# Kernel optimization log

Hardware: AMD Instinct MI355X
Metric: run time of the kernel (lower is better)

## Reference

```python
import jax, jax.numpy as jnp
import numpy as np

HID, NH_FULL, K, GAMMA = 768, 12, 9, 2
HD = HID // NH_FULL            # 64
NH = NH_FULL // GAMMA          # 6
RH = HD * NH                   # 384 reduced hidden dim
OUT_HALF = HID // 2            # 384
B, S = 8, 1024


def setup_inputs() -> dict:
    key0 = jax.random.key(0)
    ks = jax.random.split(key0, 20)
    r = lambda i, shape, sc=0.02: (jax.random.normal(ks[i], shape, dtype=jnp.float32) * sc)
    inp = {
        'query': jax.random.normal(ks[0], (B, S, HID), dtype=jnp.float32),
        'mask': jnp.ones((B, 1, 1, S), dtype=jnp.int32),
        # q/k/v projections: hidden -> reduced
        'Wq': r(1, (HID, RH)), 'bq': jnp.zeros((RH,), jnp.float32),
        'Wk': r(2, (HID, RH)), 'bk': jnp.zeros((RH,), jnp.float32),
        'Wv': r(3, (HID, RH)), 'bv': jnp.zeros((RH,), jnp.float32),
        # depthwise separable conv: depthwise [HID,1,K] + pointwise [RH,HID]
        'dw_w': r(4, (HID, 1, K), 0.1), 'dw_b': jnp.zeros((HID,), jnp.float32),
        'pw_w': r(5, (RH, HID)), 'pw_b': jnp.zeros((RH,), jnp.float32),
        # self-attn output proj: reduced -> hidden//2
        'Wsa': r(6, (RH, OUT_HALF)), 'bsa': jnp.zeros((OUT_HALF,), jnp.float32),
        # dynamic kernel layer: reduced -> K*NH
        'Wdk': r(7, (RH, K * NH)), 'bdk': jnp.zeros((K * NH,), jnp.float32),
        # dynamic attn output proj: reduced -> hidden//2
        'Wda': r(8, (RH, OUT_HALF)), 'bda': jnp.zeros((OUT_HALF,), jnp.float32),
    }
    # self_attn=True requires query==key==value
    inp['key'] = inp['query']
    inp['value'] = inp['query']
    return inp


def _forward(query, key, value, mask, Wq, bq, Wk, bk, Wv, bv,
             dw_w, dw_b, pw_w, pw_b, Wsa, bsa, Wdk, bdk, Wda, bda):
    b, s, _ = query.shape
    q = query @ Wq + bq          # [B,S,RH]
    k = key @ Wk + bk
    v = value @ Wv + bv

    # ---- depthwise separable conv over key (seq axis), 'same' padding ----
    key_t = jnp.transpose(key, (0, 2, 1))  # [B,HID,S]
    dw = jax.lax.conv_general_dilated(
        key_t, dw_w, window_strides=(1,), padding=[(K // 2, K // 2)],
        feature_group_count=HID, dimension_numbers=('NCH', 'OIH', 'NCH'))
    dw = dw + dw_b[None, :, None]          # [B,HID,S]
    ks_feat = jnp.einsum('bhs,rh->bsr', dw, pw_w) + pw_b  # [B,S,RH]

    # ---- standard multi-head self-attention branch ----
    def split(x):  # [B,S,RH] -> [B,NH,S,HD]
        return x.reshape(b, s, NH, HD).transpose(0, 2, 1, 3)
    qh, kh, vh = split(q), split(k), split(v)
    scores = jnp.einsum('bhqd,bhkd->bhqk', qh, kh) / jnp.sqrt(jnp.float32(HD))
    scores = jnp.where(mask == 0, jnp.float32(-jnp.inf), scores)
    attn_wts = jax.nn.softmax(scores, axis=-1)             # [B,NH,S,S]
    attn_out = jnp.einsum('bhqk,bhkd->bhqd', attn_wts, vh)
    attn_out = attn_out.transpose(0, 2, 1, 3).reshape(b, s, RH)
    self_out = attn_out @ Wsa + bsa                         # [B,S,HID//2]

    # ---- span dynamic conv attention branch ----
    # unfold v into sliding windows: expanded[b,s,h,d,k] = v_pad[b, s+k, h*HD+d]
    v_pad = jnp.pad(v, ((0, 0), (K // 2, K // 2), (0, 0)))  # [B,S+K-1,RH]
    windows = jnp.stack([v_pad[:, i:i + s] for i in range(K)], axis=-1)  # [B,S,RH,K]
    windows = windows.reshape(b, s, NH, HD, K)
    dyn_logits = (q * ks_feat) @ Wdk + bdk                  # [B,S,K*NH]
    dyn_kernel = jax.nn.softmax(dyn_logits.reshape(b, s, NH, K), axis=-1)
    dyn_out = jnp.einsum('bshdk,bshk->bshd', windows, dyn_kernel).reshape(b, s, RH)
    dyn_out = dyn_out @ Wda + bda                           # [B,S,HID//2]

    return attn_wts, jnp.concatenate([self_out, dyn_out], axis=-1)


def reference(query, key, value, mask, Wq, bq, Wk, bk, Wv, bv,
              dw_w, dw_b, pw_w, pw_b, Wsa, bsa, Wdk, bdk, Wda, bda):
    return _forward(query, key, value, mask, Wq, bq, Wk, bk, Wv, bv,
                    dw_w, dw_b, pw_w, pw_b, Wsa, bsa, Wdk, bdk, Wda, bda)
```

## Files before the change

### kernel.cpp

```cpp
#include <hip/hip_runtime.h>
#include <math.h>

#define B 8
#define S 1024
#define HID 768
#define RH 384
#define NH 6
#define HD 64
#define KW 9
#define KNH 54
#define OUTHALF 384
#define QLD 1152
#define EXPSCALE 0.18033688f

typedef __attribute__((ext_vector_type(8))) short short8;
typedef __attribute__((ext_vector_type(4))) float f32x4;

#define SWZ(r, c) (((r) << 6) + ((c) ^ (((r) & 7) << 3)))

__device__ __forceinline__ ushort f2bf(float x) {
    unsigned u = __float_as_uint(x);
    u += 0x7FFF + ((u >> 16) & 1);
    return (ushort)(u >> 16);
}
__device__ __forceinline__ float bf2f(ushort u) {
    return __uint_as_float(((unsigned)u) << 16);
}
__device__ __forceinline__ short8 cvt8(const float* p) {
    short8 r;
    #pragma unroll
    for (int i = 0; i < 8; i++) r[i] = (short)f2bf(p[i]);
    return r;
}

__global__ __launch_bounds__(256) void cvt_dw_fused(
    const float* __restrict__ query, const float* __restrict__ dw_w,
    const float* __restrict__ dw_b, ushort* __restrict__ Xbf,
    ushort* __restrict__ dwout)
{
    int idx = blockIdx.x*256 + threadIdx.x;
    if (idx >= B*S*(HID/8)) return;
    int c0 = (idx % (HID/8))*8;
    int s  = (idx / (HID/8)) % S;
    int b  = idx / ((HID/8)*S);

    float ctr[8];
    *(float4*)&ctr[0] = *(const float4*)(query + ((size_t)b*S + s)*HID + c0);
    *(float4*)&ctr[4] = *(const float4*)(query + ((size_t)b*S + s)*HID + c0 + 4);
    *(short8*)(Xbf + ((size_t)b*S + s)*HID + c0) = cvt8(ctr);

    float acc[8];
    *(float4*)&acc[0] = *(const float4*)(dw_b + c0);
    *(float4*)&acc[4] = *(const float4*)(dw_b + c0 + 4);
    #pragma unroll
    for (int kk = 0; kk < KW; kk++) {
        int sp = s + kk - KW/2;
        if (sp >= 0 && sp < S) {
            float row[8];
            *(float4*)&row[0] = *(const float4*)(query + ((size_t)b*S + sp)*HID + c0);
            *(float4*)&row[4] = *(const float4*)(query + ((size_t)b*S + sp)*HID + c0 + 4);
            #pragma unroll
            for (int j = 0; j < 8; j++)
                acc[j] += row[j] * dw_w[(c0+j)*KW + kk];
        }
    }
    *(short8*)(dwout + ((size_t)b*S + s)*HID + c0) = cvt8(acc);
}

__global__ __launch_bounds__(256) void prep_weights(
    const float* __restrict__ Wq, const float* __restrict__ Wk, const float* __restrict__ Wv,
    const float* __restrict__ bq, const float* __restrict__ bk, const float* __restrict__ bv,
    const float* __restrict__ pw_w, const float* __restrict__ Wsa,
    const float* __restrict__ Wda, const float* __restrict__ Wdk,
    ushort* __restrict__ WqkvT, ushort* __restrict__ pw_bf,
    ushort* __restrict__ WsaT, ushort* __restrict__ WdaT, ushort* __restrict__ WdkT,
    float* __restrict__ bqkv)
{
    int i = blockIdx.x*256 + threadIdx.x;
    if (i < 884736) {
        int n = i / 768, kk = i % 768;
        int w = n / 384, nn = n % 384;
        const float* W = (w == 0) ? Wq : (w == 1) ? Wk : Wv;
        WqkvT[i] = f2bf(W[kk*384 + nn]);
        return;
    }
    i -= 884736;
    if (i < 294912) { pw_bf[i] = f2bf(pw_w[i]); return; }
    i -= 294912;
    if (i < 147456) {
        int n = i / 384, kk = i % 384;
        WsaT[i] = f2bf(Wsa[kk*384 + n]);
        return;
    }
    i -= 147456;
    if (i < 147456) {
        int n = i / 384, kk = i % 384;
        WdaT[i] = f2bf(Wda[kk*384 + n]);
        return;
    }
    i -= 147456;
    if (i < 49152) {
        int n = i / 384, kk = i % 384;
        WdkT[i] = (n < KNH) ? f2bf(Wdk[kk*KNH + n]) : (ushort)0;
        return;
    }
    i -= 49152;
    if (i < 1152) {
        bqkv[i] = (i < 384) ? bq[i] : (i < 768) ? bk[i-384] : bv[i-768];
    }
}

template<bool OUTBF>
__global__ __launch_bounds__(256) void gemm_mfma(
    const ushort* __restrict__ A, const ushort* __restrict__ Bt,
    const float* __restrict__ bias, void* __restrict__ Cout,
    int N, int Kd, int ldc)
{
    __shared__ __attribute__((aligned(16))) ushort As[128*32];
    __shared__ __attribute__((aligned(16))) ushort Bs[128*32];
    const int t = threadIdx.x;
    const int wave = t >> 6, lane = t & 63;
    const int lr = lane & 15, lg = lane >> 4;
    const int wr = wave >> 1, wc = wave & 1;
    const int bm = blockIdx.y * 128, bn = blockIdx.x * 128;

    f32x4 acc[4][4] = {};
    const int srow = t >> 1, sseg = t & 1;
    const ushort* Arow = A + (size_t)(bm + srow)*Kd + sseg*16;
    const ushort* Brow = Bt + (size_t)(bn + srow)*Kd + sseg*16;
    const int g0 = (sseg*2) ^ (srow & 3), g1 = (sseg*2 + 1) ^ (srow & 3);
    const int swz = lg ^ (lr & 3);

    short8 av0 = *(const short8*)(Arow);
    short8 av1 = *(const short8*)(Arow + 8);
    short8 bv0 = *(const short8*)(Brow);
    short8 bv1 = *(const short8*)(Brow + 8);

    for (int k0 = 0; k0 < Kd; k0 += 32) {
        __syncthreads();
        *(short8*)&As[srow*32 + g0*8] = av0;
        *(short8*)&As[srow*32 + g1*8] = av1;
        *(short8*)&Bs[srow*32 + g0*8] = bv0;
        *(short8*)&Bs[srow*32 + g1*8] = bv1;
        __syncthreads();
        if (k0 + 32 < Kd) {
            av0 = *(const short8*)(Arow + k0 + 32);
            av1 = *(const short8*)(Arow + k0 + 40);
            bv0 = *(const short8*)(Brow + k0 + 32);
            bv1 = *(const short8*)(Brow + k0 + 40);
        }
        short8 af[4], bfr[4];
        #pragma unroll
        for (int m = 0; m < 4; m++)
            af[m] = *(const short8*)&As[(wr*64 + m*16 + lr)*32 + swz*8];
        #pragma unroll
        for (int n = 0; n < 4; n++)
            bfr[n] = *(const short8*)&Bs[(wc*64 + n*16 + lr)*32 + swz*8];
        #pragma unroll
        for (int m = 0; m < 4; m++)
            #pragma unroll
            for (int n = 0; n < 4; n++)
                acc[m][n] = __builtin_amdgcn_mfma_f32_16x16x32_bf16(af[m], bfr[n], acc[m][n], 0, 0, 0);
    }

    #pragma unroll
    for (int m = 0; m < 4; m++) {
        #pragma unroll
        for (int n = 0; n < 4; n++) {
            int gcol = bn + wc*64 + n*16 + lr;
            if (gcol >= N) continue;
            float bz = bias[gcol];
            #pragma unroll
            for (int r = 0; r < 4; r++) {
                size_t grow = bm + wr*64 + m*16 + lg*4 + r;
                float val = acc[m][n][r] + bz;
                if (OUTBF) ((ushort*)Cout)[grow*ldc + gcol] = f2bf(val);
                else       ((float*)Cout)[grow*ldc + gcol] = val;
            }
        }
    }
}

template<bool OUTBF, bool DUAL>
__global__ __launch_bounds__(256) void gemm64(
    const ushort* __restrict__ A0, const ushort* __restrict__ Bt0,
    const float* __restrict__ bias0, void* __restrict__ C0,
    const ushort* __restrict__ A1, const ushort* __restrict__ Bt1,
    const float* __restrict__ bias1,
    int N, int Kd, int ldc)
{
    __shared__ __attribute__((aligned(16))) ushort As[64*32];
    __shared__ __attribute__((aligned(16))) ushort Bs[64*32];
    const ushort* A  = (DUAL && blockIdx.z) ? A1 : A0;
    const ushort* Bt = (DUAL && blockIdx.z) ? Bt1 : Bt0;
    const float* bias = (DUAL && blockIdx.z) ? bias1 : bias0;
    const int coff = (DUAL && blockIdx.z) ? OUTHALF : 0;

    const int t = threadIdx.x;
    const int wave = t >> 6, lane = t & 63;
    const int lr = lane & 15, lg = lane >> 4;
    const int wr = wave >> 1, wc = wave & 1;
    const int bm = blockIdx.y * 64, bn = blockIdx.x * 64;

    f32x4 acc[2][2] = {};
    const int srow = t >> 2, sseg = t & 3;
    const ushort* Arow = A + (size_t)(bm + srow)*Kd + sseg*8;
    const ushort* Brow = Bt + (size_t)(bn + srow)*Kd + sseg*8;
    const int gs = sseg ^ (srow & 3);
    const int swz = lg ^ (lr & 3);

    short8 av = *(const short8*)(Arow);
    short8 bv = *(const short8*)(Brow);

    for (int k0 = 0; k0 < Kd; k0 += 32) {
        __syncthreads();
        *(short8*)&As[srow*32 + gs*8] = av;
        *(short8*)&Bs[srow*32 + gs*8] = bv;
        __syncthreads();
        if (k0 + 32 < Kd) {
            av = *(const short8*)(Arow + k0 + 32);
            bv = *(const short8*)(Brow + k0 + 32);
        }
        short8 af[2], bfr[2];
        #pragma unroll
        for (int m = 0; m < 2; m++)
            af[m] = *(const short8*)&As[(wr*32 + m*16 + lr)*32 + swz*8];
        #pragma unroll
        for (int n = 0; n < 2; n++)
            bfr[n] = *(const short8*)&Bs[(wc*32 + n*16 + lr)*32 + swz*8];
        #pragma unroll
        for (int m = 0; m < 2; m++)
            #pragma unroll
            for (int n = 0; n < 2; n++)
                acc[m][n] = __builtin_amdgcn_mfma_f32_16x16x32_bf16(af[m], bfr[n], acc[m][n], 0, 0, 0);
    }

    #pragma unroll
    for (int m = 0; m < 2; m++) {
        #pragma unroll
        for (int n = 0; n < 2; n++) {
            int gcol = bn + wc*32 + n*16 + lr;
            if (gcol >= N) continue;
            float bz = bias[gcol];
            #pragma unroll
            for (int r = 0; r < 4; r++) {
                size_t grow = bm + wr*32 + m*16 + lg*4 + r;
                float val = acc[m][n][r] + bz;
                if (OUTBF) ((ushort*)C0)[grow*ldc + gcol + coff] = f2bf(val);
                else       ((float*)C0)[grow*ldc + gcol + coff] = val;
            }
        }
    }
}

__global__ __launch_bounds__(64) void gemm_qksdk(
    const ushort* __restrict__ qkv, const ushort* __restrict__ ksf,
    const ushort* __restrict__ WdkT, const float* __restrict__ bdk,
    float* __restrict__ dynlog)
{
    const int lane = threadIdx.x;
    const int lr = lane & 15, lg = lane >> 4;
    const int r0 = blockIdx.x * 16;
    const int row = r0 + lr;

    f32x4 acc[4] = {};
    for (int ks = 0; ks < RH/32; ks++) {
        int k0 = ks*32 + lg*8;
        short8 qv = *(const short8*)(qkv + (size_t)row*QLD + k0);
        short8 kv = *(const short8*)(ksf + (size_t)row*RH + k0);
        short8 afr;
        #pragma unroll
        for (int j = 0; j < 8; j++)
            afr[j] = (short)f2bf(bf2f((ushort)qv[j]) * bf2f((ushort)kv[j]));
        #pragma unroll
        for (int t4 = 0; t4 < 4; t4++) {
            short8 bfr = *(const short8*)(WdkT + (size_t)(t4*16 + lr)*RH + k0);
            acc[t4] = __builtin_amdgcn_mfma_f32_16x16x32_bf16(afr, bfr, acc[t4], 0, 0, 0);
        }
    }
    #pragma unroll
    for (int t4 = 0; t4 < 4; t4++) {
        int n = t4*16 + lr;
        if (n >= KNH) continue;
        float bz = bdk[n];
        #pragma unroll
        for (int r = 0; r < 4; r++)
            dynlog[(size_t)(r0 + lg*4 + r)*KNH + n] = acc[t4][r] + bz;
    }
}

__global__ __launch_bounds__(256) void attn_fused(
    const ushort* __restrict__ qkv, const int* __restrict__ mask,
    float* __restrict__ out0, ushort* __restrict__ attnws)
{
    __shared__ __attribute__((aligned(16))) ushort Ks[64*64];
    __shared__ __attribute__((aligned(16))) ushort Vt[64*64];
    __shared__ __attribute__((aligned(16))) ushort Ps[4][16*64];

    const int b = blockIdx.z, h = blockIdx.y, q0 = blockIdx.x * 64;
    const int t = threadIdx.x;
    const int wave = t >> 6, lane = t & 63;
    const int lr = lane & 15, lg = lane >> 4;

    const ushort* qrow = qkv + (size_t)(b*S + q0 + wave*16 + lr)*QLD + h*HD;
    short8 aQ0 = *(const short8*)(qrow + lg*8);
    short8 aQ1 = *(const short8*)(qrow + 32 + lg*8);

    const int srow = t >> 2;
    const int sseg = t & 3;
    const int* mrow = mask + b*S;
    const ushort* krbase = qkv + RH + (size_t)(b*S + srow)*QLD + h*HD + sseg*16;
    const ushort* vbase  = qkv + 2*RH + (size_t)b*S*QLD + h*HD + srow;

    float lsum[4] = {0.f, 0.f, 0.f, 0.f};

    short8 kv0 = *(const short8*)(krbase);
    short8 kv1 = *(const short8*)(krbase + 8);
    for (int kc = 0; kc < S; kc += 64) {
        __syncthreads();
        *(short8*)&Ks[SWZ(srow, sseg*16)]     = kv0;
        *(short8*)&Ks[SWZ(srow, sseg*16 + 8)] = kv1;
        __syncthreads();
        if (kc + 64 < S) {
            const ushort* kr = krbase + (size_t)(kc + 64)*QLD;
            kv0 = *(const short8*)(kr);
            kv1 = *(const short8*)(kr + 8);
        }
        #pragma unroll
        for (int t4 = 0; t4 < 4; t4++) {
            short8 b0 = *(const short8*)&Ks[SWZ(t4*16 + lr, lg*8)];
            short8 b1 = *(const short8*)&Ks[SWZ(t4*16 + lr, 32 + lg*8)];
            f32x4 c = {0.f, 0.f, 0.f, 0.f};
            c = __builtin_amdgcn_mfma_f32_16x16x32_bf16(aQ0, b0, c, 0, 0, 0);
            c = __builtin_amdgcn_mfma_f32_16x16x32_bf16(aQ1, b1, c, 0, 0, 0);
            float add = mrow[kc + t4*16 + lr] ? 0.f : -1e30f;
            #pragma unroll
            for (int r = 0; r < 4; r++)
                lsum[r] += exp2f(c[r]*EXPSCALE + add);
        }
    }
    #pragma unroll
    for (int r = 0; r < 4; r++) {
        #pragma unroll
        for (int off = 1; off < 16; off <<= 1)
            lsum[r] += __shfl_xor(lsum[r], off, 16);
    }
    float inv[4];
    #pragma unroll
    for (int r = 0; r < 4; r++) inv[r] = 1.f / lsum[r];

    f32x4 o[4] = {};
    ushort* Psw = &Ps[wave][0];
    const size_t obase = ((size_t)((b*NH + h)*S) + q0 + wave*16) * (size_t)S;

    kv0 = *(const short8*)(krbase);
    kv1 = *(const short8*)(krbase + 8);
    ushort vb[16];
    #pragma unroll
    for (int i = 0; i < 16; i++)
        vb[i] = vbase[(size_t)(sseg*16 + i)*QLD];

    for (int kc = 0; kc < S; kc += 64) {
        __syncthreads();
        *(short8*)&Ks[SWZ(srow, sseg*16)]     = kv0;
        *(short8*)&Ks[SWZ(srow, sseg*16 + 8)] = kv1;
        *(short8*)&Vt[SWZ(srow, sseg*16)]     = *(short8*)&vb[0];
        *(short8*)&Vt[SWZ(srow, sseg*16 + 8)] = *(short8*)&vb[8];
        __syncthreads();
        if (kc + 64 < S) {
            const ushort* kr = krbase + (size_t)(kc + 64)*QLD;
            kv0 = *(const short8*)(kr);
            kv1 = *(const short8*)(kr + 8);
            const ushort* vp = vbase + (size_t)(kc + 64)*QLD;
            #pragma unroll
            for (int i = 0; i < 16; i++)
                vb[i] = vp[(size_t)(sseg*16 + i)*QLD];
        }

        #pragma unroll
        for (int t4 = 0; t4 < 4; t4++) {
            short8 b0 = *(const short8*)&Ks[SWZ(t4*16 + lr, lg*8)];
            short8 b1 = *(const short8*)&Ks[SWZ(t4*16 + lr, 32 + lg*8)];
            f32x4 c = {0.f, 0.f, 0.f, 0.f};
            c = __builtin_amdgcn_mfma_f32_16x16x32_bf16(aQ0, b0, c, 0, 0, 0);
            c = __builtin_amdgcn_mfma_f32_16x16x32_bf16(aQ1, b1, c, 0, 0, 0);
            float add = mrow[kc + t4*16 + lr] ? 0.f : -1e30f;
            #pragma unroll
            for (int r = 0; r < 4; r++) {
                float p = exp2f(c[r]*EXPSCALE + add) * inv[r];
                __builtin_nontemporal_store(p, &out0[obase + (size_t)(lg*4 + r)*S + kc + t4*16 + lr]);
                Psw[SWZ(lg*4 + r, t4*16 + lr)] = f2bf(p);
            }
        }
        #pragma unroll
        for (int kh = 0; kh < 2; kh++) {
            short8 pa = *(const short8*)&Psw[SWZ(lr, kh*32 + lg*8)];
            #pragma unroll
            for (int dt = 0; dt < 4; dt++) {
                short8 vv = *(const short8*)&Vt[SWZ(dt*16 + lr, kh*32 + lg*8)];
                o[dt] = __builtin_amdgcn_mfma_f32_16x16x32_bf16(pa, vv, o[dt], 0, 0, 0);
            }
        }
    }

    #pragma unroll
    for (int dt = 0; dt < 4; dt++)
        #pragma unroll
        for (int r = 0; r < 4; r++)
            attnws[(size_t)(b*S + q0 + wave*16 + lg*4 + r)*RH + h*HD + dt*16 + lr] = f2bf(o[dt][r]);
}

__global__ __launch_bounds__(256) void dyn_conv(
    const float* __restrict__ logits, const ushort* __restrict__ qkv,
    ushort* __restrict__ dynout)
{
    int idx = blockIdx.x*256 + threadIdx.x;
    if (idx >= B*S*(RH/4)) return;
    int r4 = (idx % (RH/4))*4;
    int s  = (idx / (RH/4)) % S;
    int b  = idx / ((RH/4)*S);
    int h  = r4 / HD;
    const float* lg = logits + ((size_t)b*S + s)*KNH + h*KW;
    float mx = lg[0];
    #pragma unroll
    for (int kk = 1; kk < KW; kk++) mx = fmaxf(mx, lg[kk]);
    float e[KW], sum = 0.f;
    #pragma unroll
    for (int kk = 0; kk < KW; kk++) { e[kk] = __expf(lg[kk]-mx); sum += e[kk]; }
    float inv = 1.f/sum;
    float acc[4] = {0.f, 0.f, 0.f, 0.f};
    const ushort* vbase = qkv + 2*RH;
    #pragma unroll
    for (int kk = 0; kk < KW; kk++) {
        int sp = s + kk - KW/2;
        if (sp >= 0 && sp < S) {
            const ushort* vp = vbase + (size_t)(b*S + sp)*QLD + r4;
            #pragma unroll
            for (int j = 0; j < 4; j++) acc[j] += bf2f(vp[j]) * e[kk];
        }
    }
    ushort4 o;
    o.x = f2bf(acc[0]*inv); o.y = f2bf(acc[1]*inv);
    o.z = f2bf(acc[2]*inv); o.w = f2bf(acc[3]*inv);
    *(ushort4*)(dynout + ((size_t)b*S + s)*RH + r4) = o;
}

extern "C" void kernel_launch(void* const* d_in, const int* in_sizes, int n_in,
                              void* d_out, int out_size, void* d_ws, size_t ws_size,
                              hipStream_t stream) {
    const float* query = (const float*)d_in[0];
    const int*   mask  = (const int*)d_in[1];
    const float* Wq    = (const float*)d_in[2];
    const float* bq    = (const float*)d_in[3];
    const float* Wk    = (const float*)d_in[4];
    const float* bk    = (const float*)d_in[5];
    const float* Wv    = (const float*)d_in[6];
    const float* bv    = (const float*)d_in[7];
    const float* dw_w  = (const float*)d_in[8];
    const float* dw_b  = (const float*)d_in[9];
    const float* pw_w  = (const float*)d_in[10];
    const float* pw_b  = (const float*)d_in[11];
    const float* Wsa   = (const float*)d_in[12];
    const float* bsa   = (const float*)d_in[13];
    const float* Wdk   = (const float*)d_in[14];
    const float* bdk   = (const float*)d_in[15];
    const float* Wda   = (const float*)d_in[16];
    const float* bda   = (const float*)d_in[17];

    float* out0 = (float*)d_out;
    float* out1 = out0 + (size_t)B*NH*S*S;

    char* wsb = (char*)d_ws;
    size_t off = 0;
    auto alloc = [&](size_t bytes) { char* p = wsb + off; off += (bytes + 255) & ~255ull; return p; };
    ushort* Xbf    = (ushort*)alloc((size_t)B*S*HID*2);
    ushort* qkvbf  = (ushort*)alloc((size_t)B*S*QLD*2);
    ushort* dwbf   = (ushort*)alloc((size_t)B*S*HID*2);
    ushort* ksf    = (ushort*)alloc((size_t)B*S*RH*2);
    ushort* attnbf = (ushort*)alloc((size_t)B*S*RH*2);
    ushort* dynbf  = (ushort*)alloc((size_t)B*S*RH*2);
    float*  dynlog = (float*) alloc((size_t)B*S*KNH*4);
    ushort* WqkvT  = (ushort*)alloc((size_t)QLD*HID*2);
    ushort* pw_bf  = (ushort*)alloc((size_t)RH*HID*2);
    ushort* WsaT   = (ushort*)alloc((size_t)RH*RH*2);
    ushort* WdaT   = (ushort*)alloc((size_t)RH*RH*2);
    ushort* WdkT   = (ushort*)alloc((size_t)128*RH*2);
    float*  bqkv   = (float*) alloc((size_t)QLD*4);

    const int M = B*S;

    prep_weights<<<(1524864 + 255)/256, 256, 0, stream>>>(
        Wq, Wk, Wv, bq, bk, bv, pw_w, Wsa, Wda, Wdk,
        WqkvT, pw_bf, WsaT, WdaT, WdkT, bqkv);

    cvt_dw_fused<<<(M*(HID/8) + 255)/256, 256, 0, stream>>>(query, dw_w, dw_b, Xbf, dwbf);

    gemm_mfma<true><<<dim3(QLD/128, M/128), 256, 0, stream>>>(
        Xbf, WqkvT, bqkv, qkvbf, QLD, HID, QLD);

    gemm64<true, false><<<dim3(RH/64, M/64), 256, 0, stream>>>(
        dwbf, pw_bf, pw_b, ksf, nullptr, nullptr, nullptr, RH, HID, RH);

    attn_fused<<<dim3(S/64, NH, B), 256, 0, stream>>>(qkvbf, mask, out0, attnbf);

    gemm_qksdk<<<M/16, 64, 0, stream>>>(qkvbf, ksf, WdkT, bdk, dynlog);

    dyn_conv<<<(M*(RH/4) + 255)/256, 256, 0, stream>>>(dynlog, qkvbf, dynbf);

    gemm64<false, true><<<dim3(OUTHALF/64, M/64, 2), 256, 0, stream>>>(
        attnbf, WsaT, bsa, out1, dynbf, WdaT, bda, OUTHALF, RH, HID);
}
```

Baseline: 303.5 us.

## Load K/B fragments directly from global, double-buffer LDS, remap attention grid

In gemm64 the B operand fragments are now read straight from global memory into registers, and only A is staged in a double-buffered LDS tile, leaving one barrier per iteration. In attn_fused the K tile is no longer staged in LDS: each lane reads its K fragment directly from global memory, V is double-buffered in LDS with a single sync per chunk, and the grid becomes 1D with a block-index swizzle that spreads (b,h) tiles across XCDs. The aim is to cut LDS traffic and barrier stalls, at the cost of more uncoalesced global/L2 reads for the K and B fragments.

```diff
diff --git a/kernel.cpp b/kernel.cpp
--- a/kernel.cpp
+++ b/kernel.cpp
@@ -189,8 +189,7 @@
     const float* __restrict__ bias1,
     int N, int Kd, int ldc)
 {
-    __shared__ __attribute__((aligned(16))) ushort As[64*32];
-    __shared__ __attribute__((aligned(16))) ushort Bs[64*32];
+    __shared__ __attribute__((aligned(16))) ushort As[2][64*32];
     const ushort* A  = (DUAL && blockIdx.z) ? A1 : A0;
     const ushort* Bt = (DUAL && blockIdx.z) ? Bt1 : Bt0;
     const float* bias = (DUAL && blockIdx.z) ? bias1 : bias0;
@@ -205,34 +204,33 @@
     f32x4 acc[2][2] = {};
     const int srow = t >> 2, sseg = t & 3;
     const ushort* Arow = A + (size_t)(bm + srow)*Kd + sseg*8;
-    const ushort* Brow = Bt + (size_t)(bn + srow)*Kd + sseg*8;
     const int gs = sseg ^ (srow & 3);
     const int swz = lg ^ (lr & 3);
+    const ushort* Br0 = Bt + (size_t)(bn + wc*32 + lr)*Kd + lg*8;
+    const ushort* Br1 = Br0 + (size_t)16*Kd;
 
     short8 av = *(const short8*)(Arow);
-    short8 bv = *(const short8*)(Brow);
+    *(short8*)&As[0][srow*32 + gs*8] = av;
+    __syncthreads();
+    int cur = 0;
 
     for (int k0 = 0; k0 < Kd; k0 += 32) {
+        if (k0 + 32 < Kd) av = *(const short8*)(Arow + k0 + 32);
+        short8 bfr0 = *(const short8*)(Br0 + k0);
+        short8 bfr1 = *(const short8*)(Br1 + k0);
+        short8 af[2];
+        #pragma unroll
+        for (int m = 0; m < 2; m++)
+            af[m] = *(const short8*)&As[cur][(wr*32 + m*16 + lr)*32 + swz*8];
+        #pragma unroll
+        for (int m = 0; m < 2; m++) {
+            acc[m][0] = __builtin_amdgcn_mfma_f32_16x16x32_bf16(af[m], bfr0, acc[m][0], 0, 0, 0);
+            acc[m][1] = __builtin_amdgcn_mfma_f32_16x16x32_bf16(af[m], bfr1, acc[m][1], 0, 0, 0);
+        }
+        if (k0 + 32 < Kd)
+            *(short8*)&As[cur^1][srow*32 + gs*8] = av;
         __syncthreads();
-        *(short8*)&As[srow*32 + gs*8] = av;
-        *(short8*)&Bs[srow*32 + gs*8] = bv;
-        __syncthreads();
-        if (k0 + 32 < Kd) {
-            av = *(const short8*)(Arow + k0 + 32);
-            bv = *(const short8*)(Brow + k0 + 32);
-        }
-        short8 af[2], bfr[2];
-        #pragma unroll
-        for (int m = 0; m < 2; m++)
-            af[m] = *(const short8*)&As[(wr*32 + m*16 + lr)*32 + swz*8];
-        #pragma unroll
-        for (int n = 0; n < 2; n++)
-            bfr[n] = *(const short8*)&Bs[(wc*32 + n*16 + lr)*32 + swz*8];
-        #pragma unroll
-        for (int m = 0; m < 2; m++)
-            #pragma unroll
-            for (int n = 0; n < 2; n++)
-                acc[m][n] = __builtin_amdgcn_mfma_f32_16x16x32_bf16(af[m], bfr[n], acc[m][n], 0, 0, 0);
+        cur ^= 1;
     }
 
     #pragma unroll
@@ -293,11 +291,15 @@
     const ushort* __restrict__ qkv, const int* __restrict__ mask,
     float* __restrict__ out0, ushort* __restrict__ attnws)
 {
-    __shared__ __attribute__((aligned(16))) ushort Ks[64*64];
-    __shared__ __attribute__((aligned(16))) ushort Vt[64*64];
+    __shared__ __attribute__((aligned(16))) ushort Vt[2][64*64];
     __shared__ __attribute__((aligned(16))) ushort Ps[4][16*64];
 
-    const int b = blockIdx.z, h = blockIdx.y, q0 = blockIdx.x * 64;
+    const int bid = blockIdx.x;
+    const int wg = (bid & 7)*96 + (bid >> 3);
+    const int q0 = (wg & 15)*64;
+    const int h  = (wg >> 4) % NH;
+    const int b  = wg / 96;
+
     const int t = threadIdx.x;
     const int wave = t >> 6, lane = t & 63;
     const int lr = lane & 15, lg = lane >> 4;
@@ -309,27 +311,17 @@
     const int srow = t >> 2;
     const int sseg = t & 3;
     const int* mrow = mask + b*S;
-    const ushort* krbase = qkv + RH + (size_t)(b*S + srow)*QLD + h*HD + sseg*16;
-    const ushort* vbase  = qkv + 2*RH + (size_t)b*S*QLD + h*HD + srow;
+    const ushort* kfrag = qkv + RH + h*HD + (size_t)b*S*QLD;
+    const ushort* vbase = qkv + 2*RH + (size_t)b*S*QLD + h*HD + srow;
 
     float lsum[4] = {0.f, 0.f, 0.f, 0.f};
 
-    short8 kv0 = *(const short8*)(krbase);
-    short8 kv1 = *(const short8*)(krbase + 8);
     for (int kc = 0; kc < S; kc += 64) {
-        __syncthreads();
-        *(short8*)&Ks[SWZ(srow, sseg*16)]     = kv0;
-        *(short8*)&Ks[SWZ(srow, sseg*16 + 8)] = kv1;
-        __syncthreads();
-        if (kc + 64 < S) {
-            const ushort* kr = krbase + (size_t)(kc + 64)*QLD;
-            kv0 = *(const short8*)(kr);
-            kv1 = *(const short8*)(kr + 8);
-        }
         #pragma unroll
         for (int t4 = 0; t4 < 4; t4++) {
-            short8 b0 = *(const short8*)&Ks[SWZ(t4*16 + lr, lg*8)];
-            short8 b1 = *(const short8*)&Ks[SWZ(t4*16 + lr, 32 + lg*8)];
+            const ushort* kr = kfrag + (size_t)(kc + t4*16 + lr)*QLD + lg*8;
+            short8 b0 = *(const short8*)(kr);
+            short8 b1 = *(const short8*)(kr + 32);
             f32x4 c = {0.f, 0.f, 0.f, 0.f};
             c = __builtin_amdgcn_mfma_f32_16x16x32_bf16(aQ0, b0, c, 0, 0, 0);
             c = __builtin_amdgcn_mfma_f32_16x16x32_bf16(aQ1, b1, c, 0, 0, 0);
@@ -353,24 +345,20 @@
     ushort* Psw = &Ps[wave][0];
     const size_t obase = ((size_t)((b*NH + h)*S) + q0 + wave*16) * (size_t)S;
 
-    kv0 = *(const short8*)(krbase);
-    kv1 = *(const short8*)(krbase + 8);
-    ushort vb[16];
-    #pragma unroll
-    for (int i = 0; i < 16; i++)
-        vb[i] = vbase[(size_t)(sseg*16 + i)*QLD];
+    {
+        ushort vb[16];
+        #pragma unroll
+        for (int i = 0; i < 16; i++)
+            vb[i] = vbase[(size_t)(sseg*16 + i)*QLD];
+        *(short8*)&Vt[0][SWZ(srow, sseg*16)]     = *(short8*)&vb[0];
+        *(short8*)&Vt[0][SWZ(srow, sseg*16 + 8)] = *(short8*)&vb[8];
+    }
+    __syncthreads();
+    int cur = 0;
 
     for (int kc = 0; kc < S; kc += 64) {
-        __syncthreads();
-        *(short8*)&Ks[SWZ(srow, sseg*16)]     = kv0;
-        *(short8*)&Ks[SWZ(srow, sseg*16 + 8)] = kv1;
-        *(short8*)&Vt[SWZ(srow, sseg*16)]     = *(short8*)&vb[0];
-        *(short8*)&Vt[SWZ(srow, sseg*16 + 8)] = *(short8*)&vb[8];
-        __syncthreads();
+        ushort vb[16];
         if (kc + 64 < S) {
-            const ushort* kr = krbase + (size_t)(kc + 64)*QLD;
-            kv0 = *(const short8*)(kr);
-            kv1 = *(const short8*)(kr + 8);
             const ushort* vp = vbase + (size_t)(kc + 64)*QLD;
             #pragma unroll
             for (int i = 0; i < 16; i++)
@@ -379,8 +367,9 @@
 
         #pragma unroll
         for (int t4 = 0; t4 < 4; t4++) {
-            short8 b0 = *(const short8*)&Ks[SWZ(t4*16 + lr, lg*8)];
-            short8 b1 = *(const short8*)&Ks[SWZ(t4*16 + lr, 32 + lg*8)];
+            const ushort* kr = kfrag + (size_t)(kc + t4*16 + lr)*QLD + lg*8;
+            short8 b0 = *(const short8*)(kr);
+            short8 b1 = *(const short8*)(kr + 32);
             f32x4 c = {0.f, 0.f, 0.f, 0.f};
             c = __builtin_amdgcn_mfma_f32_16x16x32_bf16(aQ0, b0, c, 0, 0, 0);
             c = __builtin_amdgcn_mfma_f32_16x16x32_bf16(aQ1, b1, c, 0, 0, 0);
@@ -397,10 +386,16 @@
             short8 pa = *(const short8*)&Psw[SWZ(lr, kh*32 + lg*8)];
             #pragma unroll
             for (int dt = 0; dt < 4; dt++) {
-                short8 vv = *(const short8*)&Vt[SWZ(dt*16 + lr, kh*32 + lg*8)];
+                short8 vv = *(const short8*)&Vt[cur][SWZ(dt*16 + lr, kh*32 + lg*8)];
                 o[dt] = __builtin_amdgcn_mfma_f32_16x16x32_bf16(pa, vv, o[dt], 0, 0, 0);
             }
         }
+        if (kc + 64 < S) {
+            *(short8*)&Vt[cur^1][SWZ(srow, sseg*16)]     = *(short8*)&vb[0];
+            *(short8*)&Vt[cur^1][SWZ(srow, sseg*16 + 8)] = *(short8*)&vb[8];
+        }
+        __syncthreads();
+        cur ^= 1;
     }
 
     #pragma unroll
@@ -501,7 +496,7 @@
     gemm64<true, false><<<dim3(RH/64, M/64), 256, 0, stream>>>(
         dwbf, pw_bf, pw_b, ksf, nullptr, nullptr, nullptr, RH, HID, RH);
 
-    attn_fused<<<dim3(S/64, NH, B), 256, 0, stream>>>(qkvbf, mask, out0, attnbf);
+    attn_fused<<<dim3(768), 256, 0, stream>>>(qkvbf, mask, out0, attnbf);
 
     gemm_qksdk<<<M/16, 64, 0, stream>>>(qkvbf, ksf, WdkT, bdk, dynlog);
 
```

Result: slower. 345.3 us (+13.7%).

## Split fused attention into score pass and PV pass via bf16 intermediate

Applied to the files above, without the earlier changes.

Replaces the two-pass fused attention (recomputing QK^T twice) with a score kernel that computes unnormalized exp scores once, writes them as bf16 to a global buffer plus per-row inverse sums, and a second kernel that reads them back, normalizes, writes the fp32 attention weights and does the PV MFMA. Both kernels add double-buffered LDS with one barrier per iteration. This removes the duplicate QK^T MFMA and exp work but adds a 100MB-scale bf16 write and read of the probability matrix. The fp32 weights output also changes because they are now rounded to bf16 before normalization.

```diff
diff --git a/kernel.cpp b/kernel.cpp
--- a/kernel.cpp
+++ b/kernel.cpp
@@ -289,12 +289,11 @@
     }
 }
 
-__global__ __launch_bounds__(256) void attn_fused(
+__global__ __launch_bounds__(256) void attn_scores(
     const ushort* __restrict__ qkv, const int* __restrict__ mask,
-    float* __restrict__ out0, ushort* __restrict__ attnws)
-{
-    __shared__ __attribute__((aligned(16))) ushort Ks[64*64];
-    __shared__ __attribute__((aligned(16))) ushort Vt[64*64];
+    ushort* __restrict__ Praw, float* __restrict__ invbuf)
+{
+    __shared__ __attribute__((aligned(16))) ushort Ks[2][64*64];
     __shared__ __attribute__((aligned(16))) ushort Ps[4][16*64];
 
     const int b = blockIdx.z, h = blockIdx.y, q0 = blockIdx.x * 64;
@@ -306,71 +305,121 @@
     short8 aQ0 = *(const short8*)(qrow + lg*8);
     short8 aQ1 = *(const short8*)(qrow + 32 + lg*8);
 
-    const int srow = t >> 2;
-    const int sseg = t & 3;
+    const int srow = t >> 2, sseg = t & 3;
     const int* mrow = mask + b*S;
     const ushort* krbase = qkv + RH + (size_t)(b*S + srow)*QLD + h*HD + sseg*16;
-    const ushort* vbase  = qkv + 2*RH + (size_t)b*S*QLD + h*HD + srow;
+    ushort* Psw = &Ps[wave][0];
+    const size_t prow0 = (size_t)(b*NH + h)*S + q0 + wave*16;
 
     float lsum[4] = {0.f, 0.f, 0.f, 0.f};
 
-    short8 kv0 = *(const short8*)(krbase);
-    short8 kv1 = *(const short8*)(krbase + 8);
+    {
+        short8 k0v = *(const short8*)(krbase);
+        short8 k1v = *(const short8*)(krbase + 8);
+        *(short8*)&Ks[0][SWZ(srow, sseg*16)]     = k0v;
+        *(short8*)&Ks[0][SWZ(srow, sseg*16 + 8)] = k1v;
+    }
+    __syncthreads();
+    int cur = 0;
+
     for (int kc = 0; kc < S; kc += 64) {
-        __syncthreads();
-        *(short8*)&Ks[SWZ(srow, sseg*16)]     = kv0;
-        *(short8*)&Ks[SWZ(srow, sseg*16 + 8)] = kv1;
-        __syncthreads();
+        short8 nk0, nk1;
         if (kc + 64 < S) {
             const ushort* kr = krbase + (size_t)(kc + 64)*QLD;
-            kv0 = *(const short8*)(kr);
-            kv1 = *(const short8*)(kr + 8);
+            nk0 = *(const short8*)(kr);
+            nk1 = *(const short8*)(kr + 8);
         }
         #pragma unroll
         for (int t4 = 0; t4 < 4; t4++) {
-            short8 b0 = *(const short8*)&Ks[SWZ(t4*16 + lr, lg*8)];
-            short8 b1 = *(const short8*)&Ks[SWZ(t4*16 + lr, 32 + lg*8)];
+            short8 b0 = *(const short8*)&Ks[cur][SWZ(t4*16 + lr, lg*8)];
+            short8 b1 = *(const short8*)&Ks[cur][SWZ(t4*16 + lr, 32 + lg*8)];
             f32x4 c = {0.f, 0.f, 0.f, 0.f};
             c = __builtin_amdgcn_mfma_f32_16x16x32_bf16(aQ0, b0, c, 0, 0, 0);
             c = __builtin_amdgcn_mfma_f32_16x16x32_bf16(aQ1, b1, c, 0, 0, 0);
             float add = mrow[kc + t4*16 + lr] ? 0.f : -1e30f;
             #pragma unroll
-            for (int r = 0; r < 4; r++)
-                lsum[r] += exp2f(c[r]*EXPSCALE + add);
-        }
-    }
+            for (int r = 0; r < 4; r++) {
+                float p = exp2f(c[r]*EXPSCALE + add);
+                lsum[r] += p;
+                Psw[SWZ(lg*4 + r, t4*16 + lr)] = f2bf(p);
+            }
+        }
+        {
+            int row = lane & 15, seg = lane >> 4;
+            short8 p0 = *(const short8*)&Psw[SWZ(row, seg*16)];
+            short8 p1 = *(const short8*)&Psw[SWZ(row, seg*16 + 8)];
+            ushort* gp = Praw + (prow0 + row)*S + kc + seg*16;
+            *(short8*)gp       = p0;
+            *(short8*)(gp + 8) = p1;
+        }
+        if (kc + 64 < S) {
+            *(short8*)&Ks[cur^1][SWZ(srow, sseg*16)]     = nk0;
+            *(short8*)&Ks[cur^1][SWZ(srow, sseg*16 + 8)] = nk1;
+        }
+        __syncthreads();
+        cur ^= 1;
+    }
+
     #pragma unroll
     for (int r = 0; r < 4; r++) {
         #pragma unroll
         for (int off = 1; off < 16; off <<= 1)
             lsum[r] += __shfl_xor(lsum[r], off, 16);
     }
-    float inv[4];
-    #pragma unroll
-    for (int r = 0; r < 4; r++) inv[r] = 1.f / lsum[r];
+    if (lr == 0) {
+        #pragma unroll
+        for (int r = 0; r < 4; r++)
+            invbuf[prow0 + lg*4 + r] = 1.f / lsum[r];
+    }
+}
+
+__global__ __launch_bounds__(256) void attn_pv(
+    const ushort* __restrict__ qkv, const ushort* __restrict__ Praw,
+    const float* __restrict__ invbuf, float* __restrict__ out0,
+    ushort* __restrict__ attnbf)
+{
+    __shared__ __attribute__((aligned(16))) ushort Pt[2][64*64];
+    __shared__ __attribute__((aligned(16))) ushort Vt[2][64*64];
+
+    const int b = blockIdx.z, h = blockIdx.y, q0 = blockIdx.x * 64;
+    const int t = threadIdx.x;
+    const int wave = t >> 6, lane = t & 63;
+    const int lr = lane & 15, lg = lane >> 4;
+    const int srow = t >> 2, sseg = t & 3;
+
+    const size_t rbase = (size_t)(b*NH + h)*S + q0;
+    const ushort* prbase = Praw + (rbase + srow)*S + sseg*16;
+    const ushort* vbase  = qkv + 2*RH + (size_t)b*S*QLD + h*HD + srow;
+
+    const float inv_c = invbuf[rbase + wave*16 + lr];
+    float inv_o[4];
+    #pragma unroll
+    for (int r = 0; r < 4; r++) inv_o[r] = invbuf[rbase + wave*16 + lg*4 + r];
+
+    {
+        short8 p0 = *(const short8*)(prbase);
+        short8 p1 = *(const short8*)(prbase + 8);
+        ushort vb[16];
+        #pragma unroll
+        for (int i = 0; i < 16; i++)
+            vb[i] = vbase[(size_t)(sseg*16 + i)*QLD];
+        *(short8*)&Pt[0][SWZ(srow, sseg*16)]     = p0;
+        *(short8*)&Pt[0][SWZ(srow, sseg*16 + 8)] = p1;
+        *(short8*)&Vt[0][SWZ(srow, sseg*16)]     = *(short8*)&vb[0];
+        *(short8*)&Vt[0][SWZ(srow, sseg*16 + 8)] = *(short8*)&vb[8];
+    }
+    __syncthreads();
+    int cur = 0;
 
     f32x4 o[4] = {};
-    ushort* Psw = &Ps[wave][0];
-    const size_t obase = ((size_t)((b*NH + h)*S) + q0 + wave*16) * (size_t)S;
-
-    kv0 = *(const short8*)(krbase);
-    kv1 = *(const short8*)(krbase + 8);
-    ushort vb[16];
-    #pragma unroll
-    for (int i = 0; i < 16; i++)
-        vb[i] = vbase[(size_t)(sseg*16 + i)*QLD];
+    const size_t orow = (rbase + wave*16 + lr)*(size_t)S;
 
     for (int kc = 0; kc < S; kc += 64) {
-        __syncthreads();
-        *(short8*)&Ks[SWZ(srow, sseg*16)]     = kv0;
-        *(short8*)&Ks[SWZ(srow, sseg*16 + 8)] = kv1;
-        *(short8*)&Vt[SWZ(srow, sseg*16)]     = *(short8*)&vb[0];
-        *(short8*)&Vt[SWZ(srow, sseg*16 + 8)] = *(short8*)&vb[8];
-        __syncthreads();
+        short8 np0, np1;
+        ushort vb[16];
         if (kc + 64 < S) {
-            const ushort* kr = krbase + (size_t)(kc + 64)*QLD;
-            kv0 = *(const short8*)(kr);
-            kv1 = *(const short8*)(kr + 8);
+            np0 = *(const short8*)(prbase + kc + 64);
+            np1 = *(const short8*)(prbase + kc + 72);
             const ushort* vp = vbase + (size_t)(kc + 64)*QLD;
             #pragma unroll
             for (int i = 0; i < 16; i++)
@@ -378,36 +427,37 @@
         }
 
         #pragma unroll
-        for (int t4 = 0; t4 < 4; t4++) {
-            short8 b0 = *(const short8*)&Ks[SWZ(t4*16 + lr, lg*8)];
-            short8 b1 = *(const short8*)&Ks[SWZ(t4*16 + lr, 32 + lg*8)];
-            f32x4 c = {0.f, 0.f, 0.f, 0.f};
-            c = __builtin_amdgcn_mfma_f32_16x16x32_bf16(aQ0, b0, c, 0, 0, 0);
-            c = __builtin_amdgcn_mfma_f32_16x16x32_bf16(aQ1, b1, c, 0, 0, 0);
-            float add = mrow[kc + t4*16 + lr] ? 0.f : -1e30f;
-            #pragma unroll
-            for (int r = 0; r < 4; r++) {
-                float p = exp2f(c[r]*EXPSCALE + add) * inv[r];
-                __builtin_nontemporal_store(p, &out0[obase + (size_t)(lg*4 + r)*S + kc + t4*16 + lr]);
-                Psw[SWZ(lg*4 + r, t4*16 + lr)] = f2bf(p);
-            }
-        }
-        #pragma unroll
         for (int kh = 0; kh < 2; kh++) {
-            short8 pa = *(const short8*)&Psw[SWZ(lr, kh*32 + lg*8)];
+            short8 pa = *(const short8*)&Pt[cur][SWZ(wave*16 + lr, kh*32 + lg*8)];
+            float pf[8];
+            #pragma unroll
+            for (int j = 0; j < 8; j++) pf[j] = bf2f((ushort)pa[j]) * inv_c;
+            float* op = out0 + orow + kc + kh*32 + lg*8;
+            __builtin_nontemporal_store(*(f32x4*)&pf[0], (f32x4*)op);
+            __builtin_nontemporal_store(*(f32x4*)&pf[4], (f32x4*)(op + 4));
             #pragma unroll
             for (int dt = 0; dt < 4; dt++) {
-                short8 vv = *(const short8*)&Vt[SWZ(dt*16 + lr, kh*32 + lg*8)];
+                short8 vv = *(const short8*)&Vt[cur][SWZ(dt*16 + lr, kh*32 + lg*8)];
                 o[dt] = __builtin_amdgcn_mfma_f32_16x16x32_bf16(pa, vv, o[dt], 0, 0, 0);
             }
         }
+
+        if (kc + 64 < S) {
+            *(short8*)&Pt[cur^1][SWZ(srow, sseg*16)]     = np0;
+            *(short8*)&Pt[cur^1][SWZ(srow, sseg*16 + 8)] = np1;
+            *(short8*)&Vt[cur^1][SWZ(srow, sseg*16)]     = *(short8*)&vb[0];
+            *(short8*)&Vt[cur^1][SWZ(srow, sseg*16 + 8)] = *(short8*)&vb[8];
+        }
+        __syncthreads();
+        cur ^= 1;
     }
 
     #pragma unroll
     for (int dt = 0; dt < 4; dt++)
         #pragma unroll
         for (int r = 0; r < 4; r++)
-            attnws[(size_t)(b*S + q0 + wave*16 + lg*4 + r)*RH + h*HD + dt*16 + lr] = f2bf(o[dt][r]);
+            attnbf[(size_t)(b*S + q0 + wave*16 + lg*4 + r)*RH + h*HD + dt*16 + lr] =
+                f2bf(o[dt][r] * inv_o[r]);
 }
 
 __global__ __launch_bounds__(256) void dyn_conv(
@@ -486,6 +536,8 @@
     ushort* WdaT   = (ushort*)alloc((size_t)RH*RH*2);
     ushort* WdkT   = (ushort*)alloc((size_t)128*RH*2);
     float*  bqkv   = (float*) alloc((size_t)QLD*4);
+    ushort* Praw   = (ushort*)alloc((size_t)B*NH*S*S*2);
+    float*  invbuf = (float*) alloc((size_t)B*NH*S*4);
 
     const int M = B*S;
 
@@ -501,7 +553,8 @@
     gemm64<true, false><<<dim3(RH/64, M/64), 256, 0, stream>>>(
         dwbf, pw_bf, pw_b, ksf, nullptr, nullptr, nullptr, RH, HID, RH);
 
-    attn_fused<<<dim3(S/64, NH, B), 256, 0, stream>>>(qkvbf, mask, out0, attnbf);
+    attn_scores<<<dim3(S/64, NH, B), 256, 0, stream>>>(qkvbf, mask, Praw, invbuf);
+    attn_pv<<<dim3(S/64, NH, B), 256, 0, stream>>>(qkvbf, Praw, invbuf, out0, attnbf);
 
     gemm_qksdk<<<M/16, 64, 0, stream>>>(qkvbf, ksf, WdkT, bdk, dynlog);
 
```

New measurement: 299.7 us, median of 3. Within noise of the previous version (-1.3%).
